# Performance work log

Hardware: AMD Instinct MI355X
Metric: run time of the kernel (lower is better)

## Reference

```python
import jax, jax.numpy as jnp
from jax import lax
import numpy as np

H = 256  # hidden size, hardcoded in the torch module


def setup_inputs() -> dict:
    key = jax.random.key(0)
    ks = jax.random.split(key, 7)
    B, T, D, C = 256, 512, 64, 10
    s = 1.0 / np.sqrt(H)  # torch default LSTM init scale
    return {
        "x": jax.random.normal(ks[0], (B, T, D), dtype=jnp.float32),
        "W_ih": jax.random.uniform(ks[1], (4 * H, D), jnp.float32, -s, s),
        "W_hh": jax.random.uniform(ks[2], (4 * H, H), jnp.float32, -s, s),
        "b_ih": jax.random.uniform(ks[3], (4 * H,), jnp.float32, -s, s),
        "b_hh": jax.random.uniform(ks[4], (4 * H,), jnp.float32, -s, s),
        "W_out": jax.random.uniform(ks[5], (C, H), jnp.float32, -s, s),
        "b_out": jax.random.uniform(ks[6], (C,), jnp.float32, -s, s),
    }


def reference(x, W_ih, W_hh, b_ih, b_hh, W_out, b_out):
    B, T, D = x.shape
    # Precompute the input projection for all timesteps in one big GEMM: [T, B, 4H]
    xz = jnp.einsum("btd,gd->tbg", x, W_ih) + (b_ih + b_hh)

    def step(carry, xz_t):
        h, c = carry
        z = xz_t + h @ W_hh.T  # [B, 4H]; torch gate order: i, f, g, o
        i, f, g, o = jnp.split(z, 4, axis=-1)
        c = jax.nn.sigmoid(f) * c + jax.nn.sigmoid(i) * jnp.tanh(g)
        h = jax.nn.sigmoid(o) * jnp.tanh(c)
        return (h, c), None

    h0 = jnp.zeros((B, H), x.dtype)
    (hT, _), _ = lax.scan(step, (h0, h0), xz)
    # x[:, -1, :] == final hidden state; dropout is identity at inference
    logits = hT @ W_out.T + b_out
    return jax.nn.sigmoid(logits)  # num_class > 1 branch
```

## Files before the change

kernel.cpp:

```cpp
#include <hip/hip_runtime.h>
#include <hip/hip_bf16.h>

#define Tt  512
#define Dd  64
#define CC  10

typedef short  short8 __attribute__((ext_vector_type(8)));
typedef __bf16 bf16x8 __attribute__((ext_vector_type(8)));
typedef float  f32x4  __attribute__((ext_vector_type(4)));
typedef int    int4v  __attribute__((ext_vector_type(4)));

__device__ __forceinline__ unsigned short f2bf(float f) {
    unsigned u = __builtin_bit_cast(unsigned, f);
    u += 0x7fffu + ((u >> 16) & 1u);
    return (unsigned short)(u >> 16);
}
__device__ __forceinline__ float bf2f(unsigned short s) {
    unsigned u = ((unsigned)s) << 16;
    return __builtin_bit_cast(float, u);
}
__device__ __forceinline__ float sigf(float x) {
    return __builtin_amdgcn_rcpf(1.0f + __expf(-x));
}
__device__ __forceinline__ float tanh_fast(float x) {
    return 1.0f - 2.0f * __builtin_amdgcn_rcpf(1.0f + __expf(2.0f * x));
}

__global__ void prep_weights(const float* __restrict__ W_ih,
                             const float* __restrict__ W_hh,
                             unsigned short* __restrict__ Wc) {
    int id = blockIdx.x * blockDim.x + threadIdx.x;
    int j    = id & 7;
    int lane = (id >> 3) & 63;
    int rest = id >> 9;
    int ks   = rest % 10;
    int nf   = rest / 10;
    int k    = ks * 32 + ((lane >> 4) << 3) + j;
    int row  = lane & 15;
    int h16  = nf >> 2;
    int g    = nf & 3;
    int n_orig = g * 256 + h16 * 16 + row;
    float v = (k < 256) ? W_hh[n_orig * 256 + k]
                        : W_ih[n_orig * 64 + (k - 256)];
    Wc[id] = f2bf(v);
}

__global__ void prep_bias(const float* __restrict__ b_ih,
                          const float* __restrict__ b_hh,
                          float* __restrict__ biasp) {
    int tid = blockIdx.x * blockDim.x + threadIdx.x;
    if (tid < 1024) {
        int h16 = tid >> 6, g = (tid >> 4) & 3, i = tid & 15;
        int n_orig = g * 256 + h16 * 16 + i;
        biasp[tid] = b_ih[n_orig] + b_hh[n_orig];
    }
}

__global__ __launch_bounds__(256, 1) void lstm_persist(
    const float* __restrict__ x,
    const unsigned short* __restrict__ Wc,
    const float* __restrict__ biasp,
    unsigned short* __restrict__ h0buf,
    unsigned short* __restrict__ h1buf,
    unsigned int* __restrict__ arrive,
    const float* __restrict__ W_out,
    const float* __restrict__ b_out,
    float* __restrict__ out)
{
    const int tid  = threadIdx.x;
    const int lane = tid & 63;
    const int w    = tid >> 6;
    const int bg   = blockIdx.x & 15;
    const int p    = blockIdx.x >> 4;
    const int l15  = lane & 15;
    const int lhi  = lane >> 4;

    const int h16   = p * 4 + w;
    const int batch = bg * 16 + l15;

    unsigned int* cnt  = arrive + bg * 32;
    const float*  xrow = x + (size_t)batch * (Tt * Dd) + lhi * 8;

    bf16x8 wfrag[10][4];
    #pragma unroll
    for (int ks = 0; ks < 10; ++ks)
        #pragma unroll
        for (int g = 0; g < 4; ++g)
            wfrag[ks][g] = __builtin_bit_cast(bf16x8,
                *reinterpret_cast<const short8*>(
                    Wc + (((h16 * 4 + g) * 10 + ks) * 64 + lane) * 8));
    f32x4 bias_r[4];
    #pragma unroll
    for (int g = 0; g < 4; ++g)
        bias_r[g] = __builtin_bit_cast(f32x4,
            *reinterpret_cast<const float4*>(biasp + h16 * 64 + g * 16 + lhi * 4));

    float4 xq0 = *reinterpret_cast<const float4*>(xrow);
    float4 xq1 = *reinterpret_cast<const float4*>(xrow + 4);
    float4 xq2 = *reinterpret_cast<const float4*>(xrow + 32);
    float4 xq3 = *reinterpret_cast<const float4*>(xrow + 36);

    f32x4 creg = (f32x4){0.f, 0.f, 0.f, 0.f};

    for (int t = 0; t < Tt; ++t) {
        f32x4 acc[4];
        #pragma unroll
        for (int g = 0; g < 4; ++g) acc[g] = bias_r[g];
        {
            short8 a8 = (short8){ (short)f2bf(xq0.x), (short)f2bf(xq0.y),
                                  (short)f2bf(xq0.z), (short)f2bf(xq0.w),
                                  (short)f2bf(xq1.x), (short)f2bf(xq1.y),
                                  (short)f2bf(xq1.z), (short)f2bf(xq1.w) };
            short8 a9 = (short8){ (short)f2bf(xq2.x), (short)f2bf(xq2.y),
                                  (short)f2bf(xq2.z), (short)f2bf(xq2.w),
                                  (short)f2bf(xq3.x), (short)f2bf(xq3.y),
                                  (short)f2bf(xq3.z), (short)f2bf(xq3.w) };
            bf16x8 bv8 = __builtin_bit_cast(bf16x8, a8);
            bf16x8 bv9 = __builtin_bit_cast(bf16x8, a9);
            #pragma unroll
            for (int g = 0; g < 4; ++g) {
                acc[g] = __builtin_amdgcn_mfma_f32_16x16x32_bf16(wfrag[8][g], bv8, acc[g], 0, 0, 0);
                acc[g] = __builtin_amdgcn_mfma_f32_16x16x32_bf16(wfrag[9][g], bv9, acc[g], 0, 0, 0);
            }
        }

        if (t > 0) {
            const unsigned target = 4u * (unsigned)t;
            if (lane == 0) {
                while (__hip_atomic_load(cnt, __ATOMIC_RELAXED,
                                         __HIP_MEMORY_SCOPE_AGENT) < target) {}
            }
            __builtin_amdgcn_sched_barrier(0);
            const unsigned short* hin = (t & 1) ? h1buf : h0buf;
            const void* haddr = hin + batch * 256 + lhi * 8;
            int4v h0, h1, h2, h3, h4, h5, h6, h7;
            asm volatile(
                "global_load_dwordx4 %0, %8, off sc0 sc1\n\t"
                "global_load_dwordx4 %1, %8, off offset:64 sc0 sc1\n\t"
                "global_load_dwordx4 %2, %8, off offset:128 sc0 sc1\n\t"
                "global_load_dwordx4 %3, %8, off offset:192 sc0 sc1\n\t"
                "global_load_dwordx4 %4, %8, off offset:256 sc0 sc1\n\t"
                "global_load_dwordx4 %5, %8, off offset:320 sc0 sc1\n\t"
                "global_load_dwordx4 %6, %8, off offset:384 sc0 sc1\n\t"
                "global_load_dwordx4 %7, %8, off offset:448 sc0 sc1\n\t"
                "s_waitcnt vmcnt(0)"
                : "=&v"(h0), "=&v"(h1), "=&v"(h2), "=&v"(h3),
                  "=&v"(h4), "=&v"(h5), "=&v"(h6), "=&v"(h7)
                : "v"(haddr)
                : "memory");
            int4v hvv[8] = { h0, h1, h2, h3, h4, h5, h6, h7 };
            #pragma unroll
            for (int ks = 0; ks < 8; ++ks) {
                bf16x8 bv = __builtin_bit_cast(bf16x8, hvv[ks]);
                #pragma unroll
                for (int g = 0; g < 4; ++g)
                    acc[g] = __builtin_amdgcn_mfma_f32_16x16x32_bf16(
                        wfrag[ks][g], bv, acc[g], 0, 0, 0);
            }
        }

        unsigned short* hout = ((t + 1) & 1) ? h1buf : h0buf;
        unsigned long long hpack = 0;
        #pragma unroll
        for (int r = 0; r < 4; ++r) {
            float cn = sigf(acc[1][r]) * creg[r] + sigf(acc[0][r]) * tanh_fast(acc[2][r]);
            float hn = sigf(acc[3][r]) * tanh_fast(cn);
            creg[r] = cn;
            hpack |= (unsigned long long)f2bf(hn) << (16 * r);
        }
        {
            unsigned long long* hp = reinterpret_cast<unsigned long long*>(
                hout + batch * 256 + h16 * 16 + lhi * 4);
            (void)__hip_atomic_exchange(hp, hpack, __ATOMIC_RELAXED,
                                        __HIP_MEMORY_SCOPE_AGENT);
        }

        if (t + 1 < Tt) {
            const float* xp = xrow + (size_t)(t + 1) * Dd;
            xq0 = *reinterpret_cast<const float4*>(xp);
            xq1 = *reinterpret_cast<const float4*>(xp + 4);
            xq2 = *reinterpret_cast<const float4*>(xp + 32);
            xq3 = *reinterpret_cast<const float4*>(xp + 36);
        }

        __syncthreads();
        if (tid == 0) {
            __hip_atomic_fetch_add(cnt, 1u, __ATOMIC_RELAXED,
                                   __HIP_MEMORY_SCOPE_AGENT);
        }
    }

    if (p == 0) {
        if (lane == 0) {
            while (__hip_atomic_load(cnt, __ATOMIC_RELAXED,
                                     __HIP_MEMORY_SCOPE_AGENT) < 4u * Tt) {}
        }
        __builtin_amdgcn_fence(__ATOMIC_ACQUIRE, "agent");
        const unsigned short* hT = h0buf;
        #pragma unroll 1
        for (int rr = 0; rr < 4; ++rr) {
            int row = bg * 16 + w * 4 + rr;
            ushort4 hu = *reinterpret_cast<const ushort4*>(hT + row * 256 + lane * 4);
            float f0 = bf2f(hu.x), f1 = bf2f(hu.y), f2 = bf2f(hu.z), f3 = bf2f(hu.w);
            #pragma unroll 1
            for (int cls = 0; cls < CC; ++cls) {
                float4 wv = *reinterpret_cast<const float4*>(W_out + cls * 256 + lane * 4);
                float pr = f0 * wv.x + f1 * wv.y + f2 * wv.z + f3 * wv.w;
                #pragma unroll
                for (int off = 32; off > 0; off >>= 1) pr += __shfl_down(pr, off);
                if (lane == 0) out[row * CC + cls] = sigf(pr + b_out[cls]);
            }
        }
    }
}

extern "C" void kernel_launch(void* const* d_in, const int* in_sizes, int n_in,
                              void* d_out, int out_size, void* d_ws, size_t ws_size,
                              hipStream_t stream) {
    const float* x     = (const float*)d_in[0];
    const float* W_ih  = (const float*)d_in[1];
    const float* W_hh  = (const float*)d_in[2];
    const float* b_ih  = (const float*)d_in[3];
    const float* b_hh  = (const float*)d_in[4];
    const float* W_out = (const float*)d_in[5];
    const float* b_out = (const float*)d_in[6];
    float* out = (float*)d_out;

    char* ws = (char*)d_ws;
    unsigned short* Wc    = (unsigned short*)(ws);
    float*          biasp = (float*)(ws + 655360);
    unsigned short* h0    = (unsigned short*)(ws + 659456);
    unsigned short* h1    = (unsigned short*)(ws + 790528);
    unsigned int*   arr   = (unsigned int*)(ws + 921600);

    hipLaunchKernelGGL(prep_weights, dim3(1280), dim3(256), 0, stream, W_ih, W_hh, Wc);
    hipLaunchKernelGGL(prep_bias,    dim3(4),    dim3(256), 0, stream, b_ih, b_hh, biasp);
    hipMemsetAsync(arr, 0, 2048, stream);

    hipLaunchKernelGGL(lstm_persist, dim3(64), dim3(256), 0, stream,
                       x, Wc, biasp, h0, h1, arr, W_out, b_out, out);
}
```

Measured before the change: 1.196 ms.

## Replace atomic counter barrier with sign-tagged hidden-state polling

```diff
diff --git a/kernel.cpp b/kernel.cpp
--- a/kernel.cpp
+++ b/kernel.cpp
@@ -45,14 +45,19 @@
     Wc[id] = f2bf(v);
 }
 
-__global__ void prep_bias(const float* __restrict__ b_ih,
-                          const float* __restrict__ b_hh,
-                          float* __restrict__ biasp) {
+__global__ void prep_bias_rs(const float* __restrict__ b_ih,
+                             const float* __restrict__ b_hh,
+                             const float* __restrict__ W_hh,
+                             float* __restrict__ biasp,
+                             float* __restrict__ rsum) {
     int tid = blockIdx.x * blockDim.x + threadIdx.x;
     if (tid < 1024) {
         int h16 = tid >> 6, g = (tid >> 4) & 3, i = tid & 15;
         int n_orig = g * 256 + h16 * 16 + i;
         biasp[tid] = b_ih[n_orig] + b_hh[n_orig];
+        float s = 0.f;
+        for (int k = 0; k < 256; ++k) s += W_hh[n_orig * 256 + k];
+        rsum[tid] = s;
     }
 }
 
@@ -60,9 +65,9 @@
     const float* __restrict__ x,
     const unsigned short* __restrict__ Wc,
     const float* __restrict__ biasp,
+    const float* __restrict__ rsum,
     unsigned short* __restrict__ h0buf,
     unsigned short* __restrict__ h1buf,
-    unsigned int* __restrict__ arrive,
     const float* __restrict__ W_out,
     const float* __restrict__ b_out,
     float* __restrict__ out)
@@ -78,8 +83,7 @@
     const int h16   = p * 4 + w;
     const int batch = bg * 16 + l15;
 
-    unsigned int* cnt  = arrive + bg * 32;
-    const float*  xrow = x + (size_t)batch * (Tt * Dd) + lhi * 8;
+    const float* xrow = x + (size_t)batch * (Tt * Dd) + lhi * 8;
 
     bf16x8 wfrag[10][4];
     #pragma unroll
@@ -89,11 +93,14 @@
             wfrag[ks][g] = __builtin_bit_cast(bf16x8,
                 *reinterpret_cast<const short8*>(
                     Wc + (((h16 * 4 + g) * 10 + ks) * 64 + lane) * 8));
-    f32x4 bias_r[4];
+    f32x4 bias_r[4], rs_r[4];
     #pragma unroll
-    for (int g = 0; g < 4; ++g)
+    for (int g = 0; g < 4; ++g) {
         bias_r[g] = __builtin_bit_cast(f32x4,
             *reinterpret_cast<const float4*>(biasp + h16 * 64 + g * 16 + lhi * 4));
+        rs_r[g] = __builtin_bit_cast(f32x4,
+            *reinterpret_cast<const float4*>(rsum + h16 * 64 + g * 16 + lhi * 4));
+    }
 
     float4 xq0 = *reinterpret_cast<const float4*>(xrow);
     float4 xq1 = *reinterpret_cast<const float4*>(xrow + 4);
@@ -103,9 +110,13 @@
     f32x4 creg = (f32x4){0.f, 0.f, 0.f, 0.f};
 
     for (int t = 0; t < Tt; ++t) {
+        const unsigned wantNeg = (unsigned)((t >> 1) & 1);
+        float corr = (t == 0) ? 0.0f : (wantNeg ? 1.0f : -1.0f);
+        f32x4 corrv = (f32x4){corr, corr, corr, corr};
         f32x4 acc[4];
         #pragma unroll
-        for (int g = 0; g < 4; ++g) acc[g] = bias_r[g];
+        for (int g = 0; g < 4; ++g) acc[g] = bias_r[g] + corrv * rs_r[g];
+
         {
             short8 a8 = (short8){ (short)f2bf(xq0.x), (short)f2bf(xq0.y),
                                   (short)f2bf(xq0.z), (short)f2bf(xq0.w),
@@ -125,30 +136,36 @@
         }
 
         if (t > 0) {
-            const unsigned target = 4u * (unsigned)t;
-            if (lane == 0) {
-                while (__hip_atomic_load(cnt, __ATOMIC_RELAXED,
-                                         __HIP_MEMORY_SCOPE_AGENT) < target) {}
-            }
-            __builtin_amdgcn_sched_barrier(0);
             const unsigned short* hin = (t & 1) ? h1buf : h0buf;
             const void* haddr = hin + batch * 256 + lhi * 8;
-            int4v h0, h1, h2, h3, h4, h5, h6, h7;
-            asm volatile(
-                "global_load_dwordx4 %0, %8, off sc0 sc1\n\t"
-                "global_load_dwordx4 %1, %8, off offset:64 sc0 sc1\n\t"
-                "global_load_dwordx4 %2, %8, off offset:128 sc0 sc1\n\t"
-                "global_load_dwordx4 %3, %8, off offset:192 sc0 sc1\n\t"
-                "global_load_dwordx4 %4, %8, off offset:256 sc0 sc1\n\t"
-                "global_load_dwordx4 %5, %8, off offset:320 sc0 sc1\n\t"
-                "global_load_dwordx4 %6, %8, off offset:384 sc0 sc1\n\t"
-                "global_load_dwordx4 %7, %8, off offset:448 sc0 sc1\n\t"
-                "s_waitcnt vmcnt(0)"
-                : "=&v"(h0), "=&v"(h1), "=&v"(h2), "=&v"(h3),
-                  "=&v"(h4), "=&v"(h5), "=&v"(h6), "=&v"(h7)
-                : "v"(haddr)
-                : "memory");
-            int4v hvv[8] = { h0, h1, h2, h3, h4, h5, h6, h7 };
+            int4v v0, v1, v2, v3, v4, v5, v6, v7;
+            for (;;) {
+                asm volatile(
+                    "global_load_dwordx4 %0, %8, off sc0 sc1\n\t"
+                    "global_load_dwordx4 %1, %8, off offset:64 sc0 sc1\n\t"
+                    "global_load_dwordx4 %2, %8, off offset:128 sc0 sc1\n\t"
+                    "global_load_dwordx4 %3, %8, off offset:192 sc0 sc1\n\t"
+                    "global_load_dwordx4 %4, %8, off offset:256 sc0 sc1\n\t"
+                    "global_load_dwordx4 %5, %8, off offset:320 sc0 sc1\n\t"
+                    "global_load_dwordx4 %6, %8, off offset:384 sc0 sc1\n\t"
+                    "global_load_dwordx4 %7, %8, off offset:448 sc0 sc1\n\t"
+                    "s_waitcnt vmcnt(0)"
+                    : "=&v"(v0), "=&v"(v1), "=&v"(v2), "=&v"(v3),
+                      "=&v"(v4), "=&v"(v5), "=&v"(v6), "=&v"(v7)
+                    : "v"(haddr)
+                    : "memory");
+                unsigned bad = 0;
+                bad |= (((unsigned)v0.y >> 31) ^ wantNeg) | (((unsigned)v0.w >> 31) ^ wantNeg);
+                bad |= (((unsigned)v1.y >> 31) ^ wantNeg) | (((unsigned)v1.w >> 31) ^ wantNeg);
+                bad |= (((unsigned)v2.y >> 31) ^ wantNeg) | (((unsigned)v2.w >> 31) ^ wantNeg);
+                bad |= (((unsigned)v3.y >> 31) ^ wantNeg) | (((unsigned)v3.w >> 31) ^ wantNeg);
+                bad |= (((unsigned)v4.y >> 31) ^ wantNeg) | (((unsigned)v4.w >> 31) ^ wantNeg);
+                bad |= (((unsigned)v5.y >> 31) ^ wantNeg) | (((unsigned)v5.w >> 31) ^ wantNeg);
+                bad |= (((unsigned)v6.y >> 31) ^ wantNeg) | (((unsigned)v6.w >> 31) ^ wantNeg);
+                bad |= (((unsigned)v7.y >> 31) ^ wantNeg) | (((unsigned)v7.w >> 31) ^ wantNeg);
+                if (!__any((int)bad)) break;
+            }
+            int4v hvv[8] = { v0, v1, v2, v3, v4, v5, v6, v7 };
             #pragma unroll
             for (int ks = 0; ks < 8; ++ks) {
                 bf16x8 bv = __builtin_bit_cast(bf16x8, hvv[ks]);
@@ -160,13 +177,14 @@
         }
 
         unsigned short* hout = ((t + 1) & 1) ? h1buf : h0buf;
+        const float bnext = (((t + 1) >> 1) & 1) ? -1.0f : 1.0f;
         unsigned long long hpack = 0;
         #pragma unroll
         for (int r = 0; r < 4; ++r) {
             float cn = sigf(acc[1][r]) * creg[r] + sigf(acc[0][r]) * tanh_fast(acc[2][r]);
             float hn = sigf(acc[3][r]) * tanh_fast(cn);
             creg[r] = cn;
-            hpack |= (unsigned long long)f2bf(hn) << (16 * r);
+            hpack |= (unsigned long long)f2bf(hn + bnext) << (16 * r);
         }
         {
             unsigned long long* hp = reinterpret_cast<unsigned long long*>(
@@ -182,26 +200,24 @@
             xq2 = *reinterpret_cast<const float4*>(xp + 32);
             xq3 = *reinterpret_cast<const float4*>(xp + 36);
         }
-
-        __syncthreads();
-        if (tid == 0) {
-            __hip_atomic_fetch_add(cnt, 1u, __ATOMIC_RELAXED,
-                                   __HIP_MEMORY_SCOPE_AGENT);
-        }
     }
 
     if (p == 0) {
-        if (lane == 0) {
-            while (__hip_atomic_load(cnt, __ATOMIC_RELAXED,
-                                     __HIP_MEMORY_SCOPE_AGENT) < 4u * Tt) {}
-        }
-        __builtin_amdgcn_fence(__ATOMIC_ACQUIRE, "agent");
-        const unsigned short* hT = h0buf;
         #pragma unroll 1
         for (int rr = 0; rr < 4; ++rr) {
             int row = bg * 16 + w * 4 + rr;
-            ushort4 hu = *reinterpret_cast<const ushort4*>(hT + row * 256 + lane * 4);
-            float f0 = bf2f(hu.x), f1 = bf2f(hu.y), f2 = bf2f(hu.z), f3 = bf2f(hu.w);
+            const void* haddr = h0buf + row * 256 + lane * 4;
+            unsigned long long hu;
+            for (;;) {
+                asm volatile(
+                    "global_load_dwordx2 %0, %1, off sc0 sc1\n\ts_waitcnt vmcnt(0)"
+                    : "=&v"(hu) : "v"(haddr) : "memory");
+                if (!__any((int)(hu >> 63))) break;
+            }
+            float f0 = bf2f((unsigned short)(hu & 0xffff)) - 1.0f;
+            float f1 = bf2f((unsigned short)((hu >> 16) & 0xffff)) - 1.0f;
+            float f2 = bf2f((unsigned short)((hu >> 32) & 0xffff)) - 1.0f;
+            float f3 = bf2f((unsigned short)(hu >> 48)) - 1.0f;
             #pragma unroll 1
             for (int cls = 0; cls < CC; ++cls) {
                 float4 wv = *reinterpret_cast<const float4*>(W_out + cls * 256 + lane * 4);
@@ -229,14 +245,16 @@
     char* ws = (char*)d_ws;
     unsigned short* Wc    = (unsigned short*)(ws);
     float*          biasp = (float*)(ws + 655360);
-    unsigned short* h0    = (unsigned short*)(ws + 659456);
-    unsigned short* h1    = (unsigned short*)(ws + 790528);
-    unsigned int*   arr   = (unsigned int*)(ws + 921600);
+    float*          rsum  = (float*)(ws + 659456);
+    unsigned short* h0    = (unsigned short*)(ws + 663552);
+    unsigned short* h1    = (unsigned short*)(ws + 794624);
 
     hipLaunchKernelGGL(prep_weights, dim3(1280), dim3(256), 0, stream, W_ih, W_hh, Wc);
-    hipLaunchKernelGGL(prep_bias,    dim3(4),    dim3(256), 0, stream, b_ih, b_hh, biasp);
-    hipMemsetAsync(arr, 0, 2048, stream);
+    hipLaunchKernelGGL(prep_bias_rs, dim3(4),    dim3(256), 0, stream,
+                       b_ih, b_hh, W_hh, biasp, rsum);
+    hipMemsetAsync(h0, 0x3F, 131072, stream);
+    hipMemsetAsync(h1, 0xBF, 131072, stream);
 
     hipLaunchKernelGGL(lstm_persist, dim3(64), dim3(256), 0, stream,
-                       x, Wc, biasp, h0, h1, arr, W_out, b_out, out);
-}
+                       x, Wc, biasp, rsum, h0, h1, W_out, b_out, out);
+}
```

Result: slower. 1.286 ms (+7.5%).

## Process four batch groups per block, shrinking the persistent grid to 16 blocks

Applied to the files above, without the earlier changes.

```diff
diff --git a/kernel.cpp b/kernel.cpp
--- a/kernel.cpp
+++ b/kernel.cpp
@@ -4,6 +4,7 @@
 #define Tt  512
 #define Dd  64
 #define CC  10
+#define NG  4
 
 typedef short  short8 __attribute__((ext_vector_type(8)));
 typedef __bf16 bf16x8 __attribute__((ext_vector_type(8)));
@@ -70,16 +71,12 @@
     const int tid  = threadIdx.x;
     const int lane = tid & 63;
     const int w    = tid >> 6;
-    const int bg   = blockIdx.x & 15;
-    const int p    = blockIdx.x >> 4;
+    const int set  = blockIdx.x & 3;
+    const int p    = blockIdx.x >> 2;
     const int l15  = lane & 15;
     const int lhi  = lane >> 4;
 
-    const int h16   = p * 4 + w;
-    const int batch = bg * 16 + l15;
-
-    unsigned int* cnt  = arrive + bg * 32;
-    const float*  xrow = x + (size_t)batch * (Tt * Dd) + lhi * 8;
+    const int h16 = p * 4 + w;
 
     bf16x8 wfrag[10][4];
     #pragma unroll
@@ -95,120 +92,138 @@
         bias_r[g] = __builtin_bit_cast(f32x4,
             *reinterpret_cast<const float4*>(biasp + h16 * 64 + g * 16 + lhi * 4));
 
-    float4 xq0 = *reinterpret_cast<const float4*>(xrow);
-    float4 xq1 = *reinterpret_cast<const float4*>(xrow + 4);
-    float4 xq2 = *reinterpret_cast<const float4*>(xrow + 32);
-    float4 xq3 = *reinterpret_cast<const float4*>(xrow + 36);
-
-    f32x4 creg = (f32x4){0.f, 0.f, 0.f, 0.f};
+    int           batch[NG];
+    const float*  xrow[NG];
+    unsigned int* cntq[NG];
+    f32x4         creg[NG];
+    float4        xq[NG][4];
+    #pragma unroll
+    for (int q = 0; q < NG; ++q) {
+        int bg   = set * NG + q;
+        batch[q] = bg * 16 + l15;
+        xrow[q]  = x + (size_t)batch[q] * (Tt * Dd) + lhi * 8;
+        cntq[q]  = arrive + bg * 32;
+        creg[q]  = (f32x4){0.f, 0.f, 0.f, 0.f};
+        xq[q][0] = *reinterpret_cast<const float4*>(xrow[q]);
+        xq[q][1] = *reinterpret_cast<const float4*>(xrow[q] + 4);
+        xq[q][2] = *reinterpret_cast<const float4*>(xrow[q] + 32);
+        xq[q][3] = *reinterpret_cast<const float4*>(xrow[q] + 36);
+    }
 
     for (int t = 0; t < Tt; ++t) {
-        f32x4 acc[4];
         #pragma unroll
-        for (int g = 0; g < 4; ++g) acc[g] = bias_r[g];
-        {
-            short8 a8 = (short8){ (short)f2bf(xq0.x), (short)f2bf(xq0.y),
-                                  (short)f2bf(xq0.z), (short)f2bf(xq0.w),
-                                  (short)f2bf(xq1.x), (short)f2bf(xq1.y),
-                                  (short)f2bf(xq1.z), (short)f2bf(xq1.w) };
-            short8 a9 = (short8){ (short)f2bf(xq2.x), (short)f2bf(xq2.y),
-                                  (short)f2bf(xq2.z), (short)f2bf(xq2.w),
-                                  (short)f2bf(xq3.x), (short)f2bf(xq3.y),
-                                  (short)f2bf(xq3.z), (short)f2bf(xq3.w) };
-            bf16x8 bv8 = __builtin_bit_cast(bf16x8, a8);
-            bf16x8 bv9 = __builtin_bit_cast(bf16x8, a9);
+        for (int q = 0; q < NG; ++q) {
+            f32x4 acc[4];
             #pragma unroll
-            for (int g = 0; g < 4; ++g) {
-                acc[g] = __builtin_amdgcn_mfma_f32_16x16x32_bf16(wfrag[8][g], bv8, acc[g], 0, 0, 0);
-                acc[g] = __builtin_amdgcn_mfma_f32_16x16x32_bf16(wfrag[9][g], bv9, acc[g], 0, 0, 0);
+            for (int g = 0; g < 4; ++g) acc[g] = bias_r[g];
+            {
+                float4 x0 = xq[q][0], x1 = xq[q][1], x2 = xq[q][2], x3 = xq[q][3];
+                short8 a8 = (short8){ (short)f2bf(x0.x), (short)f2bf(x0.y),
+                                      (short)f2bf(x0.z), (short)f2bf(x0.w),
+                                      (short)f2bf(x1.x), (short)f2bf(x1.y),
+                                      (short)f2bf(x1.z), (short)f2bf(x1.w) };
+                short8 a9 = (short8){ (short)f2bf(x2.x), (short)f2bf(x2.y),
+                                      (short)f2bf(x2.z), (short)f2bf(x2.w),
+                                      (short)f2bf(x3.x), (short)f2bf(x3.y),
+                                      (short)f2bf(x3.z), (short)f2bf(x3.w) };
+                bf16x8 bv8 = __builtin_bit_cast(bf16x8, a8);
+                bf16x8 bv9 = __builtin_bit_cast(bf16x8, a9);
+                #pragma unroll
+                for (int g = 0; g < 4; ++g) {
+                    acc[g] = __builtin_amdgcn_mfma_f32_16x16x32_bf16(wfrag[8][g], bv8, acc[g], 0, 0, 0);
+                    acc[g] = __builtin_amdgcn_mfma_f32_16x16x32_bf16(wfrag[9][g], bv9, acc[g], 0, 0, 0);
+                }
+            }
+
+            if (t > 0) {
+                const unsigned target = 4u * (unsigned)t;
+                if (lane == 0) {
+                    while (__hip_atomic_load(cntq[q], __ATOMIC_RELAXED,
+                                             __HIP_MEMORY_SCOPE_AGENT) < target) {}
+                }
+                __builtin_amdgcn_sched_barrier(0);
+                const unsigned short* hin = (t & 1) ? h1buf : h0buf;
+                const void* haddr = hin + batch[q] * 256 + lhi * 8;
+                int4v v0, v1, v2, v3, v4, v5, v6, v7;
+                asm volatile(
+                    "global_load_dwordx4 %0, %8, off sc0 sc1\n\t"
+                    "global_load_dwordx4 %1, %8, off offset:64 sc0 sc1\n\t"
+                    "global_load_dwordx4 %2, %8, off offset:128 sc0 sc1\n\t"
+                    "global_load_dwordx4 %3, %8, off offset:192 sc0 sc1\n\t"
+                    "global_load_dwordx4 %4, %8, off offset:256 sc0 sc1\n\t"
+                    "global_load_dwordx4 %5, %8, off offset:320 sc0 sc1\n\t"
+                    "global_load_dwordx4 %6, %8, off offset:384 sc0 sc1\n\t"
+                    "global_load_dwordx4 %7, %8, off offset:448 sc0 sc1\n\t"
+                    "s_waitcnt vmcnt(0)"
+                    : "=&v"(v0), "=&v"(v1), "=&v"(v2), "=&v"(v3),
+                      "=&v"(v4), "=&v"(v5), "=&v"(v6), "=&v"(v7)
+                    : "v"(haddr)
+                    : "memory");
+                int4v hvv[8] = { v0, v1, v2, v3, v4, v5, v6, v7 };
+                #pragma unroll
+                for (int ks = 0; ks < 8; ++ks) {
+                    bf16x8 bv = __builtin_bit_cast(bf16x8, hvv[ks]);
+                    #pragma unroll
+                    for (int g = 0; g < 4; ++g)
+                        acc[g] = __builtin_amdgcn_mfma_f32_16x16x32_bf16(
+                            wfrag[ks][g], bv, acc[g], 0, 0, 0);
+                }
+            }
+
+            unsigned short* hout = ((t + 1) & 1) ? h1buf : h0buf;
+            unsigned long long hpack = 0;
+            #pragma unroll
+            for (int r = 0; r < 4; ++r) {
+                float cn = sigf(acc[1][r]) * creg[q][r] + sigf(acc[0][r]) * tanh_fast(acc[2][r]);
+                float hn = sigf(acc[3][r]) * tanh_fast(cn);
+                creg[q][r] = cn;
+                hpack |= (unsigned long long)f2bf(hn) << (16 * r);
+            }
+            {
+                unsigned long long* hp = reinterpret_cast<unsigned long long*>(
+                    hout + batch[q] * 256 + h16 * 16 + lhi * 4);
+                (void)__hip_atomic_exchange(hp, hpack, __ATOMIC_RELAXED,
+                                            __HIP_MEMORY_SCOPE_AGENT);
+            }
+
+            if (t + 1 < Tt) {
+                const float* xp = xrow[q] + (size_t)(t + 1) * Dd;
+                xq[q][0] = *reinterpret_cast<const float4*>(xp);
+                xq[q][1] = *reinterpret_cast<const float4*>(xp + 4);
+                xq[q][2] = *reinterpret_cast<const float4*>(xp + 32);
+                xq[q][3] = *reinterpret_cast<const float4*>(xp + 36);
+            }
+
+            __syncthreads();
+            if (tid == 0) {
+                __hip_atomic_fetch_add(cntq[q], 1u, __ATOMIC_RELAXED,
+                                       __HIP_MEMORY_SCOPE_AGENT);
             }
         }
-
-        if (t > 0) {
-            const unsigned target = 4u * (unsigned)t;
+    }
+
+    if (p == 0) {
+        #pragma unroll 1
+        for (int q = 0; q < NG; ++q) {
             if (lane == 0) {
-                while (__hip_atomic_load(cnt, __ATOMIC_RELAXED,
-                                         __HIP_MEMORY_SCOPE_AGENT) < target) {}
-            }
-            __builtin_amdgcn_sched_barrier(0);
-            const unsigned short* hin = (t & 1) ? h1buf : h0buf;
-            const void* haddr = hin + batch * 256 + lhi * 8;
-            int4v h0, h1, h2, h3, h4, h5, h6, h7;
-            asm volatile(
-                "global_load_dwordx4 %0, %8, off sc0 sc1\n\t"
-                "global_load_dwordx4 %1, %8, off offset:64 sc0 sc1\n\t"
-                "global_load_dwordx4 %2, %8, off offset:128 sc0 sc1\n\t"
-                "global_load_dwordx4 %3, %8, off offset:192 sc0 sc1\n\t"
-                "global_load_dwordx4 %4, %8, off offset:256 sc0 sc1\n\t"
-                "global_load_dwordx4 %5, %8, off offset:320 sc0 sc1\n\t"
-                "global_load_dwordx4 %6, %8, off offset:384 sc0 sc1\n\t"
-                "global_load_dwordx4 %7, %8, off offset:448 sc0 sc1\n\t"
-                "s_waitcnt vmcnt(0)"
-                : "=&v"(h0), "=&v"(h1), "=&v"(h2), "=&v"(h3),
-                  "=&v"(h4), "=&v"(h5), "=&v"(h6), "=&v"(h7)
-                : "v"(haddr)
-                : "memory");
-            int4v hvv[8] = { h0, h1, h2, h3, h4, h5, h6, h7 };
-            #pragma unroll
-            for (int ks = 0; ks < 8; ++ks) {
-                bf16x8 bv = __builtin_bit_cast(bf16x8, hvv[ks]);
-                #pragma unroll
-                for (int g = 0; g < 4; ++g)
-                    acc[g] = __builtin_amdgcn_mfma_f32_16x16x32_bf16(
-                        wfrag[ks][g], bv, acc[g], 0, 0, 0);
-            }
-        }
-
-        unsigned short* hout = ((t + 1) & 1) ? h1buf : h0buf;
-        unsigned long long hpack = 0;
-        #pragma unroll
-        for (int r = 0; r < 4; ++r) {
-            float cn = sigf(acc[1][r]) * creg[r] + sigf(acc[0][r]) * tanh_fast(acc[2][r]);
-            float hn = sigf(acc[3][r]) * tanh_fast(cn);
-            creg[r] = cn;
-            hpack |= (unsigned long long)f2bf(hn) << (16 * r);
-        }
-        {
-            unsigned long long* hp = reinterpret_cast<unsigned long long*>(
-                hout + batch * 256 + h16 * 16 + lhi * 4);
-            (void)__hip_atomic_exchange(hp, hpack, __ATOMIC_RELAXED,
-                                        __HIP_MEMORY_SCOPE_AGENT);
-        }
-
-        if (t + 1 < Tt) {
-            const float* xp = xrow + (size_t)(t + 1) * Dd;
-            xq0 = *reinterpret_cast<const float4*>(xp);
-            xq1 = *reinterpret_cast<const float4*>(xp + 4);
-            xq2 = *reinterpret_cast<const float4*>(xp + 32);
-            xq3 = *reinterpret_cast<const float4*>(xp + 36);
-        }
-
-        __syncthreads();
-        if (tid == 0) {
-            __hip_atomic_fetch_add(cnt, 1u, __ATOMIC_RELAXED,
-                                   __HIP_MEMORY_SCOPE_AGENT);
-        }
-    }
-
-    if (p == 0) {
-        if (lane == 0) {
-            while (__hip_atomic_load(cnt, __ATOMIC_RELAXED,
-                                     __HIP_MEMORY_SCOPE_AGENT) < 4u * Tt) {}
-        }
-        __builtin_amdgcn_fence(__ATOMIC_ACQUIRE, "agent");
-        const unsigned short* hT = h0buf;
-        #pragma unroll 1
-        for (int rr = 0; rr < 4; ++rr) {
-            int row = bg * 16 + w * 4 + rr;
-            ushort4 hu = *reinterpret_cast<const ushort4*>(hT + row * 256 + lane * 4);
-            float f0 = bf2f(hu.x), f1 = bf2f(hu.y), f2 = bf2f(hu.z), f3 = bf2f(hu.w);
+                while (__hip_atomic_load(cntq[q], __ATOMIC_RELAXED,
+                                         __HIP_MEMORY_SCOPE_AGENT) < 4u * Tt) {}
+            }
+            __builtin_amdgcn_fence(__ATOMIC_ACQUIRE, "agent");
+            const unsigned short* hT = h0buf;
             #pragma unroll 1
-            for (int cls = 0; cls < CC; ++cls) {
-                float4 wv = *reinterpret_cast<const float4*>(W_out + cls * 256 + lane * 4);
-                float pr = f0 * wv.x + f1 * wv.y + f2 * wv.z + f3 * wv.w;
-                #pragma unroll
-                for (int off = 32; off > 0; off >>= 1) pr += __shfl_down(pr, off);
-                if (lane == 0) out[row * CC + cls] = sigf(pr + b_out[cls]);
+            for (int rr = 0; rr < 4; ++rr) {
+                int row = (set * NG + q) * 16 + w * 4 + rr;
+                ushort4 hu = *reinterpret_cast<const ushort4*>(hT + row * 256 + lane * 4);
+                float f0 = bf2f(hu.x), f1 = bf2f(hu.y), f2 = bf2f(hu.z), f3 = bf2f(hu.w);
+                #pragma unroll 1
+                for (int cls = 0; cls < CC; ++cls) {
+                    float4 wv = *reinterpret_cast<const float4*>(W_out + cls * 256 + lane * 4);
+                    float pr = f0 * wv.x + f1 * wv.y + f2 * wv.z + f3 * wv.w;
+                    #pragma unroll
+                    for (int off = 32; off > 0; off >>= 1) pr += __shfl_down(pr, off);
+                    if (lane == 0) out[row * CC + cls] = sigf(pr + b_out[cls]);
+                }
             }
         }
     }
@@ -237,6 +252,6 @@
     hipLaunchKernelGGL(prep_bias,    dim3(4),    dim3(256), 0, stream, b_ih, b_hh, biasp);
     hipMemsetAsync(arr, 0, 2048, stream);
 
-    hipLaunchKernelGGL(lstm_persist, dim3(64), dim3(256), 0, stream,
+    hipLaunchKernelGGL(lstm_persist, dim3(16), dim3(256), 0, stream,
                        x, Wc, biasp, h0, h1, arr, W_out, b_out, out);
 }
```

Result: slower. 4.623 ms (+286.4%).

## Split persistent LSTM into single-wave blocks with LDS-resident weight fragments

Applied to the files above, without the earlier changes.

```diff
diff --git a/kernel.cpp b/kernel.cpp
--- a/kernel.cpp
+++ b/kernel.cpp
@@ -56,7 +56,7 @@
     }
 }
 
-__global__ __launch_bounds__(256, 1) void lstm_persist(
+__global__ __launch_bounds__(64, 1) void lstm_persist(
     const float* __restrict__ x,
     const unsigned short* __restrict__ Wc,
     const float* __restrict__ biasp,
@@ -67,33 +67,31 @@
     const float* __restrict__ b_out,
     float* __restrict__ out)
 {
-    const int tid  = threadIdx.x;
-    const int lane = tid & 63;
-    const int w    = tid >> 6;
+    const int lane = threadIdx.x;
     const int bg   = blockIdx.x & 15;
-    const int p    = blockIdx.x >> 4;
+    const int pp   = blockIdx.x >> 4;
     const int l15  = lane & 15;
     const int lhi  = lane >> 4;
 
-    const int h16   = p * 4 + w;
+    const int h16   = pp;
     const int batch = bg * 16 + l15;
 
     unsigned int* cnt  = arrive + bg * 32;
     const float*  xrow = x + (size_t)batch * (Tt * Dd) + lhi * 8;
 
-    bf16x8 wfrag[10][4];
+    __shared__ unsigned short wlds[40 * 512];
+    __shared__ float          blds[64];
     #pragma unroll
     for (int ks = 0; ks < 10; ++ks)
         #pragma unroll
-        for (int g = 0; g < 4; ++g)
-            wfrag[ks][g] = __builtin_bit_cast(bf16x8,
-                *reinterpret_cast<const short8*>(
-                    Wc + (((h16 * 4 + g) * 10 + ks) * 64 + lane) * 8));
-    f32x4 bias_r[4];
-    #pragma unroll
-    for (int g = 0; g < 4; ++g)
-        bias_r[g] = __builtin_bit_cast(f32x4,
-            *reinterpret_cast<const float4*>(biasp + h16 * 64 + g * 16 + lhi * 4));
+        for (int g = 0; g < 4; ++g) {
+            uint4 v = *reinterpret_cast<const uint4*>(
+                Wc + (((h16 * 4 + g) * 10 + ks) * 64 + lane) * 8);
+            *reinterpret_cast<uint4*>(
+                reinterpret_cast<char*>(wlds) + (ks * 4 + g) * 1024 + lane * 16) = v;
+        }
+    blds[lane] = biasp[h16 * 64 + lane];
+    __syncthreads();
 
     float4 xq0 = *reinterpret_cast<const float4*>(xrow);
     float4 xq1 = *reinterpret_cast<const float4*>(xrow + 4);
@@ -102,10 +100,17 @@
 
     f32x4 creg = (f32x4){0.f, 0.f, 0.f, 0.f};
 
+    auto WF = [&](int ks, int g) -> bf16x8 {
+        return __builtin_bit_cast(bf16x8, *reinterpret_cast<const uint4*>(
+            reinterpret_cast<const char*>(wlds) + (ks * 4 + g) * 1024 + lane * 16));
+    };
+
     for (int t = 0; t < Tt; ++t) {
         f32x4 acc[4];
         #pragma unroll
-        for (int g = 0; g < 4; ++g) acc[g] = bias_r[g];
+        for (int g = 0; g < 4; ++g)
+            acc[g] = __builtin_bit_cast(f32x4,
+                *reinterpret_cast<const float4*>(&blds[g * 16 + lhi * 4]));
         {
             short8 a8 = (short8){ (short)f2bf(xq0.x), (short)f2bf(xq0.y),
                                   (short)f2bf(xq0.z), (short)f2bf(xq0.w),
@@ -119,13 +124,13 @@
             bf16x8 bv9 = __builtin_bit_cast(bf16x8, a9);
             #pragma unroll
             for (int g = 0; g < 4; ++g) {
-                acc[g] = __builtin_amdgcn_mfma_f32_16x16x32_bf16(wfrag[8][g], bv8, acc[g], 0, 0, 0);
-                acc[g] = __builtin_amdgcn_mfma_f32_16x16x32_bf16(wfrag[9][g], bv9, acc[g], 0, 0, 0);
+                acc[g] = __builtin_amdgcn_mfma_f32_16x16x32_bf16(WF(8, g), bv8, acc[g], 0, 0, 0);
+                acc[g] = __builtin_amdgcn_mfma_f32_16x16x32_bf16(WF(9, g), bv9, acc[g], 0, 0, 0);
             }
         }
 
         if (t > 0) {
-            const unsigned target = 4u * (unsigned)t;
+            const unsigned target = 16u * (unsigned)t;
             if (lane == 0) {
                 while (__hip_atomic_load(cnt, __ATOMIC_RELAXED,
                                          __HIP_MEMORY_SCOPE_AGENT) < target) {}
@@ -133,7 +138,7 @@
             __builtin_amdgcn_sched_barrier(0);
             const unsigned short* hin = (t & 1) ? h1buf : h0buf;
             const void* haddr = hin + batch * 256 + lhi * 8;
-            int4v h0, h1, h2, h3, h4, h5, h6, h7;
+            int4v v0, v1, v2, v3, v4, v5, v6, v7;
             asm volatile(
                 "global_load_dwordx4 %0, %8, off sc0 sc1\n\t"
                 "global_load_dwordx4 %1, %8, off offset:64 sc0 sc1\n\t"
@@ -144,18 +149,18 @@
                 "global_load_dwordx4 %6, %8, off offset:384 sc0 sc1\n\t"
                 "global_load_dwordx4 %7, %8, off offset:448 sc0 sc1\n\t"
                 "s_waitcnt vmcnt(0)"
-                : "=&v"(h0), "=&v"(h1), "=&v"(h2), "=&v"(h3),
-                  "=&v"(h4), "=&v"(h5), "=&v"(h6), "=&v"(h7)
+                : "=&v"(v0), "=&v"(v1), "=&v"(v2), "=&v"(v3),
+                  "=&v"(v4), "=&v"(v5), "=&v"(v6), "=&v"(v7)
                 : "v"(haddr)
                 : "memory");
-            int4v hvv[8] = { h0, h1, h2, h3, h4, h5, h6, h7 };
+            int4v hvv[8] = { v0, v1, v2, v3, v4, v5, v6, v7 };
             #pragma unroll
             for (int ks = 0; ks < 8; ++ks) {
                 bf16x8 bv = __builtin_bit_cast(bf16x8, hvv[ks]);
                 #pragma unroll
                 for (int g = 0; g < 4; ++g)
                     acc[g] = __builtin_amdgcn_mfma_f32_16x16x32_bf16(
-                        wfrag[ks][g], bv, acc[g], 0, 0, 0);
+                        WF(ks, g), bv, acc[g], 0, 0, 0);
             }
         }
 
@@ -183,23 +188,24 @@
             xq3 = *reinterpret_cast<const float4*>(xp + 36);
         }
 
-        __syncthreads();
-        if (tid == 0) {
+        asm volatile("s_waitcnt vmcnt(0)" ::: "memory");
+        __builtin_amdgcn_sched_barrier(0);
+        if (lane == 0) {
             __hip_atomic_fetch_add(cnt, 1u, __ATOMIC_RELAXED,
                                    __HIP_MEMORY_SCOPE_AGENT);
         }
     }
 
-    if (p == 0) {
+    if (pp == 0) {
         if (lane == 0) {
             while (__hip_atomic_load(cnt, __ATOMIC_RELAXED,
-                                     __HIP_MEMORY_SCOPE_AGENT) < 4u * Tt) {}
+                                     __HIP_MEMORY_SCOPE_AGENT) < 16u * Tt) {}
         }
         __builtin_amdgcn_fence(__ATOMIC_ACQUIRE, "agent");
         const unsigned short* hT = h0buf;
         #pragma unroll 1
-        for (int rr = 0; rr < 4; ++rr) {
-            int row = bg * 16 + w * 4 + rr;
+        for (int rr = 0; rr < 16; ++rr) {
+            int row = bg * 16 + rr;
             ushort4 hu = *reinterpret_cast<const ushort4*>(hT + row * 256 + lane * 4);
             float f0 = bf2f(hu.x), f1 = bf2f(hu.y), f2 = bf2f(hu.z), f3 = bf2f(hu.w);
             #pragma unroll 1
@@ -237,6 +243,6 @@
     hipLaunchKernelGGL(prep_bias,    dim3(4),    dim3(256), 0, stream, b_ih, b_hh, biasp);
     hipMemsetAsync(arr, 0, 2048, stream);
 
-    hipLaunchKernelGGL(lstm_persist, dim3(64), dim3(256), 0, stream,
+    hipLaunchKernelGGL(lstm_persist, dim3(256), dim3(64), 0, stream,
                        x, Wc, biasp, h0, h1, arr, W_out, b_out, out);
 }
```

Result: slower. 1.328 ms (+11.0%).
